# Kernel tuning notes

Measured on AMD Instinct MI355X. Metric: run time of the kernel, lower is better.

Reference implementation:

```python
import jax, jax.numpy as jnp
import numpy as np

NUM_HEADS = 12
HEAD_SIZE = 64  # hidden_size // num_heads


def setup_inputs() -> dict:
    key = jax.random.key(0)
    ks = jax.random.split(key, 4)
    B, S, H = 2, 2048, 768
    return {
        "hidden_states": jax.random.normal(ks[0], (B, S, H), dtype=jnp.float32),
        "attention_mask": jnp.ones((B, S), dtype=jnp.int32),
        "Wq": jax.random.normal(ks[1], (H, H), dtype=jnp.float32) * 0.02,
        "bq": jnp.zeros((H,), dtype=jnp.float32),
        "Wk": jax.random.normal(ks[2], (H, H), dtype=jnp.float32) * 0.02,
        "bk": jnp.zeros((H,), dtype=jnp.float32),
        "Wv": jax.random.normal(ks[3], (H, H), dtype=jnp.float32) * 0.02,
        "bv": jnp.zeros((H,), dtype=jnp.float32),
    }


def reference(hidden_states, attention_mask, Wq, bq, Wk, bk, Wv, bv):
    B, S, H = hidden_states.shape
    nh, hs = NUM_HEADS, HEAD_SIZE

    def to_heads(x):  # [B,S,H] -> [nh,B,S,hs] (matches to_multi_head)
        return x.reshape(B, S, nh, hs).transpose(2, 0, 1, 3)

    # torch Linear: y = x @ W.T + b
    q = to_heads(hidden_states @ Wq.T + bq)
    k = to_heads(hidden_states @ Wk.T + bk)
    v = to_heads(hidden_states @ Wv.T + bv)

    scores = jnp.einsum("hbqd,hbkd->hbqk", q, k) / jnp.float32(hs) ** 0.5
    # mask: 1 -> attend, 0 -> -inf; broadcast over query dim
    m = 1.0 - attention_mask.astype(scores.dtype)
    add = jnp.where(m != 0.0, -jnp.inf, 0.0)[None, :, None, :]  # [1,B,1,S]
    probs = jax.nn.softmax(scores + add, axis=-1)
    # dropout is identity in eval mode
    out = jnp.einsum("hbqk,hbkd->hbqd", probs, v)
    # from_multi_head: [nh,B,S,hs] -> [B,S,H]
    return out.transpose(1, 2, 0, 3).reshape(B, S, H)
```

## Files before the change

kernel.cpp:

```cpp
#include <hip/hip_runtime.h>
#include <hip/hip_bf16.h>

#define BATCH 2
#define SEQ   2048
#define HID   768
#define NH    12
#define HS    64
#define MROWS (BATCH*SEQ)
#define N3    (3*HID)
#define HB    (NH*BATCH)

typedef __attribute__((ext_vector_type(8))) short short8;
typedef __attribute__((ext_vector_type(4))) float floatx4;

#define QSCALE 0.1803368801111204f

__device__ __forceinline__ unsigned short f2bf(float x){
  __hip_bfloat16 h = __float2bfloat16(x);
  return __builtin_bit_cast(unsigned short, h);
}
__device__ __forceinline__ unsigned int f2bf2(float lo, float hi){
  return (unsigned int)f2bf(lo) | ((unsigned int)f2bf(hi) << 16);
}
__device__ __forceinline__ void glds16(const unsigned short* g, unsigned short* l){
  __builtin_amdgcn_global_load_lds(
    (const __attribute__((address_space(1))) unsigned int*)g,
    (__attribute__((address_space(3))) unsigned int*)l, 16, 0, 0);
}

__global__ void f2bf_all_kernel(const float* __restrict__ X,
                                const float* __restrict__ Wq,
                                const float* __restrict__ Wk,
                                const float* __restrict__ Wv,
                                const int* __restrict__ mask,
                                unsigned short* __restrict__ Xb,
                                unsigned short* __restrict__ Wb,
                                float* __restrict__ maskaddG,
                                int* __restrict__ flagsG){
  const int XQ = MROWS*HID/4;
  const int WQ = HID*HID/4;
  const int NB = (XQ + 3*WQ)/256;
  const int tid = threadIdx.x;
  if(blockIdx.x == NB){
    for(int i=tid;i<BATCH*SEQ;i+=256) maskaddG[i] = mask[i] ? 0.f : -1e30f;
    if(tid < BATCH*32){
      int b = tid >> 5, t = tid & 31;
      const int* mrow = mask + b*SEQ + t*64;
      int any = 0;
      for(int i=0;i<64;i++) any |= (mrow[i]==0);
      flagsG[tid] = any;
    }
    return;
  }
  int i = blockIdx.x * 256 + tid;
  const float* src; unsigned short* dst; int off;
  if(i < XQ){ src = X; dst = Xb; off = i; }
  else {
    int j = i - XQ;
    int w = j / WQ; off = j - w*WQ;
    src = (w==0) ? Wq : (w==1) ? Wk : Wv;
    dst = Wb + (size_t)w*HID*HID;
  }
  float4 v = reinterpret_cast<const float4*>(src)[off];
  ushort4 o;
  o.x = f2bf(v.x); o.y = f2bf(v.y); o.z = f2bf(v.z); o.w = f2bf(v.w);
  reinterpret_cast<ushort4*>(dst)[off] = o;
}

__global__ __launch_bounds__(256) void qkv_gemm_kernel(
    const unsigned short* __restrict__ Xb,
    const unsigned short* __restrict__ Wb,
    const float* __restrict__ bq, const float* __restrict__ bk, const float* __restrict__ bv,
    unsigned short* __restrict__ Qb, unsigned short* __restrict__ Kb,
    unsigned short* __restrict__ Vtb)
{
  __shared__ __align__(16) union {
    struct { unsigned short A[2][128][32]; unsigned short B[2][128][32]; } s;
    unsigned short T[4][64][72];
  } u;
  const int m0 = blockIdx.y << 7;
  const int n0 = blockIdx.x << 7;
  const int tid  = threadIdx.x;
  const int wave = tid >> 6, lane = tid & 63;
  const int wr = wave >> 1, wc = wave & 1;
  const int quad = lane >> 4, l15 = lane & 15;

  const unsigned short* gsrc[4];
  unsigned short* ldst[4];
  #pragma unroll
  for(int p=0;p<4;p++){
    int ck  = ((p&1)<<8) + tid;
    int row = ck>>2, c = ck&3, pc = c ^ (row&3);
    if(p<2){ gsrc[p] = Xb + (size_t)(m0+row)*HID + (pc<<3); ldst[p] = &u.s.A[0][row][c<<3]; }
    else   { gsrc[p] = Wb + (size_t)(n0+row)*HID + (pc<<3); ldst[p] = &u.s.B[0][row][c<<3]; }
  }

  floatx4 acc[4][4];
  #pragma unroll
  for(int i=0;i<4;i++)
    #pragma unroll
    for(int j=0;j<4;j++) acc[i][j] = (floatx4){0.f,0.f,0.f,0.f};

  auto stage = [&](int buf, int k0){
    const int bo = buf*(128*32);
    #pragma unroll
    for(int p=0;p<4;p++) glds16(gsrc[p] + k0, ldst[p] + bo);
  };

  stage(0, 0);
  __syncthreads();

  const int swa = l15 & 3;
  for(int t=0;t<HID/32;t++){
    const int buf = t & 1;
    if(t < HID/32 - 1) stage(buf^1, (t+1)*32);
    short8 a[4], b[4];
    #pragma unroll
    for(int i=0;i<4;i++)
      a[i] = *reinterpret_cast<const short8*>(&u.s.A[buf][wr*64+i*16+l15][(quad^swa)<<3]);
    #pragma unroll
    for(int j=0;j<4;j++)
      b[j] = *reinterpret_cast<const short8*>(&u.s.B[buf][wc*64+j*16+l15][(quad^swa)<<3]);
    #pragma unroll
    for(int i=0;i<4;i++)
      #pragma unroll
      for(int j=0;j<4;j++)
        acc[i][j] = __builtin_amdgcn_mfma_f32_16x16x32_bf16(a[i], b[j], acc[i][j], 0, 0, 0);
    __syncthreads();
  }

  const int which = n0 / HID;
  const int nbase = n0 - which*HID + wc*64;
  const int head  = nbase >> 6;
  const int b_    = m0 >> 11;
  const int hb    = head*BATCH + b_;
  const int s0    = (m0 & 2047) + wr*64;
  if(which < 2){
    unsigned short* dst = which==0 ? Qb : Kb;
    const float* bias = which==0 ? bq : bk;
    const float scale = which==0 ? QSCALE : 1.0f;
    #pragma unroll
    for(int j=0;j<4;j++){
      const float bb = bias[nbase + j*16 + l15];
      #pragma unroll
      for(int i=0;i<4;i++)
        #pragma unroll
        for(int r=0;r<4;r++)
          u.T[wave][i*16 + quad*4 + r][j*16 + l15] = f2bf((acc[i][j][r] + bb)*scale);
    }
    #pragma unroll
    for(int p=0;p<8;p++){
      const int row = p*8 + (lane>>3), dc = (lane&7)*8;
      uint4 v = *reinterpret_cast<const uint4*>(&u.T[wave][row][dc]);
      *reinterpret_cast<uint4*>(dst + ((size_t)(hb<<11) + s0 + row)*HS + dc) = v;
    }
  } else {
    #pragma unroll
    for(int j=0;j<4;j++){
      const float bb = bv[nbase + j*16 + l15];
      #pragma unroll
      for(int i=0;i<4;i++){
        uint2 pk;
        pk.x = f2bf2(acc[i][j][0]+bb, acc[i][j][1]+bb);
        pk.y = f2bf2(acc[i][j][2]+bb, acc[i][j][3]+bb);
        *reinterpret_cast<uint2*>(&u.T[wave][j*16+l15][i*16 + quad*4]) = pk;
      }
    }
    #pragma unroll
    for(int p=0;p<8;p++){
      const int d = p*8 + (lane>>3), cm = lane & 7;
      uint4 v = *reinterpret_cast<const uint4*>(&u.T[wave][d][cm*8]);
      *reinterpret_cast<uint4*>(Vtb + ((size_t)(hb*HS) + d)*SEQ + s0 + cm*8) = v;
    }
  }
}

__global__ __launch_bounds__(256) void attn_kernel(
    const unsigned short* __restrict__ Qb,
    const unsigned short* __restrict__ Kb,
    const unsigned short* __restrict__ Vtb,
    const float* __restrict__ maskaddG,
    const int* __restrict__ flagsG,
    float* __restrict__ out)
{
  __shared__ __align__(16) unsigned short Ks2 [2][64][64];
  __shared__ __align__(16) unsigned short Vts2[2][64][64];
  __shared__ __align__(16) unsigned short Ps2 [4][16][68];

  const int bid = blockIdx.x;
  const int hb = bid >> 5, qt = bid & 31, q0 = qt << 6;
  const int tid = threadIdx.x, wave = tid >> 6, lane = tid & 63;
  const int quad = lane >> 4, l15 = lane & 15;
  const int b_ = hb & 1, head = hb >> 1;

  const unsigned short* gK[2]; const unsigned short* gV[2];
  unsigned short* lK[2]; unsigned short* lV[2];
  #pragma unroll
  for(int p=0;p<2;p++){
    int ck = (p<<8) + tid;
    int row = ck>>3, c = ck&7, pc = c ^ (row&7);
    gK[p] = Kb  + ((size_t)(hb<<11) + row)*HS + (pc<<3);
    lK[p] = &Ks2[0][row][c<<3];
    gV[p] = Vtb + ((size_t)(hb*HS) + row)*SEQ + (pc<<3);
    lV[p] = &Vts2[0][row][c<<3];
  }
  auto stage = [&](int buf, int k0){
    const int bo = buf*(64*64);
    #pragma unroll
    for(int p=0;p<2;p++){
      glds16(gK[p] + (size_t)k0*HS, lK[p] + bo);
      glds16(gV[p] + k0,           lV[p] + bo);
    }
  };

  stage(0, 0);

  short8 a_q[2];
  {
    const unsigned short* qsrc = Qb + ((size_t)(hb<<11) + q0 + wave*16 + l15)*HS;
    a_q[0] = *reinterpret_cast<const short8*>(qsrc + quad*8);
    a_q[1] = *reinterpret_cast<const short8*>(qsrc + 32 + quad*8);
  }

  float lsum4[4] = {0.f,0.f,0.f,0.f};
  floatx4 o_acc[4];
  #pragma unroll
  for(int dt=0;dt<4;dt++) o_acc[dt] = (floatx4){0.f,0.f,0.f,0.f};

  __syncthreads();

  const int sw = l15 & 7;
  for(int t=0;t<SEQ/64;t++){
    const int buf = t & 1, k0 = t << 6;
    if(t < SEQ/64 - 1) stage(buf^1, k0 + 64);

    const unsigned short (*Kst)[64] = Ks2[buf];
    const unsigned short (*Vst)[64] = Vts2[buf];

    floatx4 st[4];
    #pragma unroll
    for(int kt=0;kt<4;kt++){
      st[kt] = (floatx4){0.f,0.f,0.f,0.f};
      #pragma unroll
      for(int c=0;c<2;c++){
        short8 kf = *reinterpret_cast<const short8*>(
            &Kst[kt*16 + l15][(((c<<2)+quad)^sw)<<3]);
        st[kt] = __builtin_amdgcn_mfma_f32_16x16x32_bf16(kf, a_q[c], st[kt], 0, 0, 0);
      }
    }

    const bool masked = (flagsG[(b_<<5) + t] != 0);
    #pragma unroll
    for(int kt=0;kt<4;kt++){
      float p0,p1,p2,p3;
      if(!masked){
        p0 = exp2f(st[kt][0]); p1 = exp2f(st[kt][1]);
        p2 = exp2f(st[kt][2]); p3 = exp2f(st[kt][3]);
      } else {
        float4 ma = *reinterpret_cast<const float4*>(
            maskaddG + (b_<<11) + k0 + kt*16 + quad*4);
        p0 = exp2f(st[kt][0] + ma.x); p1 = exp2f(st[kt][1] + ma.y);
        p2 = exp2f(st[kt][2] + ma.z); p3 = exp2f(st[kt][3] + ma.w);
      }
      lsum4[0] += p0; lsum4[1] += p1; lsum4[2] += p2; lsum4[3] += p3;
      uint2 pk;
      pk.x = f2bf2(p0, p1);
      pk.y = f2bf2(p2, p3);
      *reinterpret_cast<uint2*>(&Ps2[wave][l15][kt*16 + quad*4]) = pk;
    }

    short8 ap0, ap1;
    {
      unsigned long long x0 = *reinterpret_cast<const unsigned long long*>(&Ps2[wave][l15][quad*8]);
      unsigned long long x1 = *reinterpret_cast<const unsigned long long*>(&Ps2[wave][l15][quad*8 + 4]);
      unsigned long long y0 = *reinterpret_cast<const unsigned long long*>(&Ps2[wave][l15][32 + quad*8]);
      unsigned long long y1 = *reinterpret_cast<const unsigned long long*>(&Ps2[wave][l15][32 + quad*8 + 4]);
      union { unsigned long long u[2]; short8 s; } cv0, cv1;
      cv0.u[0] = x0; cv0.u[1] = x1;
      cv1.u[0] = y0; cv1.u[1] = y1;
      ap0 = cv0.s; ap1 = cv1.s;
    }
    #pragma unroll
    for(int dt=0;dt<4;dt++){
      short8 bv0 = *reinterpret_cast<const short8*>(&Vst[dt*16 + l15][(quad^sw)<<3]);
      short8 bv1 = *reinterpret_cast<const short8*>(&Vst[dt*16 + l15][((4+quad)^sw)<<3]);
      o_acc[dt] = __builtin_amdgcn_mfma_f32_16x16x32_bf16(ap0, bv0, o_acc[dt], 0, 0, 0);
      o_acc[dt] = __builtin_amdgcn_mfma_f32_16x16x32_bf16(ap1, bv1, o_acc[dt], 0, 0, 0);
    }
    __syncthreads();
  }

  float lsum = (lsum4[0]+lsum4[1]) + (lsum4[2]+lsum4[3]);
  lsum += __shfl_xor(lsum, 16);
  lsum += __shfl_xor(lsum, 32);
  float linv[4];
  #pragma unroll
  for(int r=0;r<4;r++) linv[r] = 1.0f / __shfl(lsum, quad*4 + r);

  #pragma unroll
  for(int dt=0;dt<4;dt++){
    #pragma unroll
    for(int r=0;r<4;r++){
      const int srow = q0 + wave*16 + quad*4 + r;
      out[((size_t)(b_<<11) + srow)*HID + (head<<6) + dt*16 + l15] =
        o_acc[dt][r] * linv[r];
    }
  }
}

extern "C" void kernel_launch(void* const* d_in, const int* in_sizes, int n_in,
                              void* d_out, int out_size, void* d_ws, size_t ws_size,
                              hipStream_t stream) {
  const float* X    = (const float*)d_in[0];
  const int*   mask = (const int*)  d_in[1];
  const float* Wq   = (const float*)d_in[2];
  const float* bq   = (const float*)d_in[3];
  const float* Wk   = (const float*)d_in[4];
  const float* bk   = (const float*)d_in[5];
  const float* Wv   = (const float*)d_in[6];
  const float* bv   = (const float*)d_in[7];
  float* out = (float*)d_out;

  char* ws = (char*)d_ws;
  unsigned short* Xb  = (unsigned short*)ws;
  unsigned short* Wb  = Xb  + (size_t)MROWS*HID;
  unsigned short* Qb  = Wb  + (size_t)N3*HID;
  unsigned short* Kb  = Qb  + (size_t)HB*SEQ*HS;
  unsigned short* Vtb = Kb  + (size_t)HB*SEQ*HS;
  float* maskaddG = (float*)(Vtb + (size_t)HB*SEQ*HS);
  int*   flagsG   = (int*)(maskaddG + MROWS);

  const int total_quads = (MROWS*HID + 3*HID*HID)/4;
  f2bf_all_kernel<<<total_quads/256 + 1, 256, 0, stream>>>(
      X, Wq, Wk, Wv, mask, Xb, Wb, maskaddG, flagsG);

  qkv_gemm_kernel<<<dim3(N3/128, MROWS/128), 256, 0, stream>>>(
      Xb, Wb, bq, bk, bv, Qb, Kb, Vtb);

  attn_kernel<<<HB*32, 256, 0, stream>>>(
      Qb, Kb, Vtb, maskaddG, flagsG, out);
}
```

Before: 175.2 us.

## Add producer wave for K/V loads with LDS flag handshakes instead of barriers

The attention kernel gets a fifth wave that acts as a dedicated producer. It streams K and V^T tiles into a double-buffered LDS area and signals readiness through workgroup-scope atomic flags. The four consumer waves spin on those flags and report completion per buffer, replacing the per-iteration __syncthreads. Mask flags are also packed into one bitmask word per batch, so each tile needs a bit test instead of a global load. The risks are spin-wait overhead, lower occupancy from 320-thread blocks, and the producer running only one tile ahead.

```diff
diff --git a/kernel.cpp b/kernel.cpp
--- a/kernel.cpp
+++ b/kernel.cpp
@@ -27,6 +27,7 @@
     (const __attribute__((address_space(1))) unsigned int*)g,
     (__attribute__((address_space(3))) unsigned int*)l, 16, 0, 0);
 }
+#define WAITCNT_VM_LGKM0() __builtin_amdgcn_s_waitcnt(0x0070)
 
 __global__ void f2bf_all_kernel(const float* __restrict__ X,
                                 const float* __restrict__ Wq,
@@ -36,19 +37,21 @@
                                 unsigned short* __restrict__ Xb,
                                 unsigned short* __restrict__ Wb,
                                 float* __restrict__ maskaddG,
-                                int* __restrict__ flagsG){
+                                unsigned int* __restrict__ flagsG){
   const int XQ = MROWS*HID/4;
   const int WQ = HID*HID/4;
   const int NB = (XQ + 3*WQ)/256;
   const int tid = threadIdx.x;
   if(blockIdx.x == NB){
     for(int i=tid;i<BATCH*SEQ;i+=256) maskaddG[i] = mask[i] ? 0.f : -1e30f;
+    if(tid < 2) flagsG[tid] = 0u;
+    __syncthreads();
     if(tid < BATCH*32){
       int b = tid >> 5, t = tid & 31;
       const int* mrow = mask + b*SEQ + t*64;
       int any = 0;
       for(int i=0;i<64;i++) any |= (mrow[i]==0);
-      flagsG[tid] = any;
+      if(any) atomicOr(&flagsG[b], 1u << t);
     }
     return;
   }
@@ -175,45 +178,56 @@
   }
 }
 
-__global__ __launch_bounds__(256) void attn_kernel(
+__global__ __launch_bounds__(320) void attn_kernel(
     const unsigned short* __restrict__ Qb,
     const unsigned short* __restrict__ Kb,
     const unsigned short* __restrict__ Vtb,
     const float* __restrict__ maskaddG,
-    const int* __restrict__ flagsG,
+    const unsigned int* __restrict__ flagsG,
     float* __restrict__ out)
 {
   __shared__ __align__(16) unsigned short Ks2 [2][64][64];
   __shared__ __align__(16) unsigned short Vts2[2][64][64];
   __shared__ __align__(16) unsigned short Ps2 [4][16][68];
+  __shared__ int ready[2];
+  __shared__ int done[2];
 
   const int bid = blockIdx.x;
   const int hb = bid >> 5, qt = bid & 31, q0 = qt << 6;
   const int tid = threadIdx.x, wave = tid >> 6, lane = tid & 63;
   const int quad = lane >> 4, l15 = lane & 15;
   const int b_ = hb & 1, head = hb >> 1;
-
-  const unsigned short* gK[2]; const unsigned short* gV[2];
-  unsigned short* lK[2]; unsigned short* lV[2];
-  #pragma unroll
-  for(int p=0;p<2;p++){
-    int ck = (p<<8) + tid;
-    int row = ck>>3, c = ck&7, pc = c ^ (row&7);
-    gK[p] = Kb  + ((size_t)(hb<<11) + row)*HS + (pc<<3);
-    lK[p] = &Ks2[0][row][c<<3];
-    gV[p] = Vtb + ((size_t)(hb*HS) + row)*SEQ + (pc<<3);
-    lV[p] = &Vts2[0][row][c<<3];
-  }
-  auto stage = [&](int buf, int k0){
-    const int bo = buf*(64*64);
-    #pragma unroll
-    for(int p=0;p<2;p++){
-      glds16(gK[p] + (size_t)k0*HS, lK[p] + bo);
-      glds16(gV[p] + k0,           lV[p] + bo);
-    }
-  };
-
-  stage(0, 0);
+  const int NT = SEQ/64;
+
+  if(tid < 2){ ready[tid] = -1; done[tid] = 0; }
+  __syncthreads();
+
+  if(wave == 4){
+    const int prow = lane >> 3;
+    const int pcol = lane & 7;
+    const int ppc  = pcol ^ prow;
+    const unsigned short* gK0 = Kb  + ((size_t)(hb<<11) + prow)*HS + (ppc<<3);
+    const unsigned short* gV0 = Vtb + ((size_t)(hb*HS) + prow)*SEQ + (ppc<<3);
+
+    for(int t=0;t<NT;t++){
+      const int b = t & 1, k0 = t << 6;
+      const int k = (t - b) >> 1;
+      if(k > 0){
+        while(__hip_atomic_load(&done[b], __ATOMIC_ACQUIRE, __HIP_MEMORY_SCOPE_WORKGROUP) < 4*k)
+          __builtin_amdgcn_s_sleep(1);
+      }
+      #pragma unroll
+      for(int p=0;p<8;p++)
+        glds16(gK0 + (size_t)(k0 + p*8)*HS, &Ks2[b][p*8 + prow][pcol*8]);
+      #pragma unroll
+      for(int p=0;p<8;p++)
+        glds16(gV0 + (size_t)(p*8)*SEQ + k0, &Vts2[b][p*8 + prow][pcol*8]);
+      WAITCNT_VM_LGKM0();
+      if(lane == 0)
+        __hip_atomic_store(&ready[b], t, __ATOMIC_RELEASE, __HIP_MEMORY_SCOPE_WORKGROUP);
+    }
+    return;
+  }
 
   short8 a_q[2];
   {
@@ -221,21 +235,21 @@
     a_q[0] = *reinterpret_cast<const short8*>(qsrc + quad*8);
     a_q[1] = *reinterpret_cast<const short8*>(qsrc + 32 + quad*8);
   }
+  const unsigned int fl = flagsG[b_];
 
   float lsum4[4] = {0.f,0.f,0.f,0.f};
   floatx4 o_acc[4];
   #pragma unroll
   for(int dt=0;dt<4;dt++) o_acc[dt] = (floatx4){0.f,0.f,0.f,0.f};
 
-  __syncthreads();
-
   const int sw = l15 & 7;
-  for(int t=0;t<SEQ/64;t++){
-    const int buf = t & 1, k0 = t << 6;
-    if(t < SEQ/64 - 1) stage(buf^1, k0 + 64);
-
-    const unsigned short (*Kst)[64] = Ks2[buf];
-    const unsigned short (*Vst)[64] = Vts2[buf];
+  for(int t=0;t<NT;t++){
+    const int b = t & 1, k0 = t << 6;
+    while(__hip_atomic_load(&ready[b], __ATOMIC_ACQUIRE, __HIP_MEMORY_SCOPE_WORKGROUP) < t)
+      __builtin_amdgcn_s_sleep(1);
+
+    const unsigned short (*Kst)[64] = Ks2[b];
+    const unsigned short (*Vst)[64] = Vts2[b];
 
     floatx4 st[4];
     #pragma unroll
@@ -249,7 +263,7 @@
       }
     }
 
-    const bool masked = (flagsG[(b_<<5) + t] != 0);
+    const bool masked = (fl >> t) & 1u;
     #pragma unroll
     for(int kt=0;kt<4;kt++){
       float p0,p1,p2,p3;
@@ -287,7 +301,10 @@
       o_acc[dt] = __builtin_amdgcn_mfma_f32_16x16x32_bf16(ap0, bv0, o_acc[dt], 0, 0, 0);
       o_acc[dt] = __builtin_amdgcn_mfma_f32_16x16x32_bf16(ap1, bv1, o_acc[dt], 0, 0, 0);
     }
-    __syncthreads();
+
+    WAITCNT_VM_LGKM0();
+    if(lane == 0)
+      __hip_atomic_fetch_add(&done[b], 1, __ATOMIC_RELEASE, __HIP_MEMORY_SCOPE_WORKGROUP);
   }
 
   float lsum = (lsum4[0]+lsum4[1]) + (lsum4[2]+lsum4[3]);
@@ -328,7 +345,7 @@
   unsigned short* Kb  = Qb  + (size_t)HB*SEQ*HS;
   unsigned short* Vtb = Kb  + (size_t)HB*SEQ*HS;
   float* maskaddG = (float*)(Vtb + (size_t)HB*SEQ*HS);
-  int*   flagsG   = (int*)(maskaddG + MROWS);
+  unsigned int* flagsG = (unsigned int*)(maskaddG + MROWS);
 
   const int total_quads = (MROWS*HID + 3*HID*HID)/4;
   f2bf_all_kernel<<<total_quads/256 + 1, 256, 0, stream>>>(
@@ -337,6 +354,6 @@
   qkv_gemm_kernel<<<dim3(N3/128, MROWS/128), 256, 0, stream>>>(
       Xb, Wb, bq, bk, bv, Qb, Kb, Vtb);
 
-  attn_kernel<<<HB*32, 256, 0, stream>>>(
+  attn_kernel<<<HB*32, 320, 0, stream>>>(
       Qb, Kb, Vtb, maskaddG, flagsG, out);
 }
```

After: 175.5 us. No clear change (+0.2%).

## Fuse bf16 conversion into QKV GEMM via grid-wide barrier, pack mask flags

Applied to the files above, without the earlier changes.

Merges the fp32-to-bf16 conversion kernel into the QKV GEMM kernel. All 576 blocks first do a grid-stride conversion, then synchronize through a global atomic spin barrier before starting the GEMM. Mask flags become one bitmask word per batch, loaded once per attention block instead of once per tile. The probability packing switches to a cheaper round-half-up bit trick. This removes a kernel launch and a per-tile global load, but the barrier only works if all 576 blocks are resident at once (launch_bounds 256,3) and adds a memset launch.

```diff
diff --git a/kernel.cpp b/kernel.cpp
--- a/kernel.cpp
+++ b/kernel.cpp
@@ -9,6 +9,7 @@
 #define MROWS (BATCH*SEQ)
 #define N3    (3*HID)
 #define HB    (NH*BATCH)
+#define NBLK_GEMM 576
 
 typedef __attribute__((ext_vector_type(8))) short short8;
 typedef __attribute__((ext_vector_type(4))) float floatx4;
@@ -21,6 +22,11 @@
 }
 __device__ __forceinline__ unsigned int f2bf2(float lo, float hi){
   return (unsigned int)f2bf(lo) | ((unsigned int)f2bf(hi) << 16);
+}
+__device__ __forceinline__ unsigned int f2bf2_rhu(float lo, float hi){
+  unsigned int a = __builtin_bit_cast(unsigned int, lo) + 0x8000u;
+  unsigned int b = __builtin_bit_cast(unsigned int, hi) + 0x8000u;
+  return __builtin_amdgcn_perm(b, a, 0x07060302u);
 }
 __device__ __forceinline__ void glds16(const unsigned short* g, unsigned short* l){
   __builtin_amdgcn_global_load_lds(
@@ -28,59 +34,69 @@
     (__attribute__((address_space(3))) unsigned int*)l, 16, 0, 0);
 }
 
-__global__ void f2bf_all_kernel(const float* __restrict__ X,
-                                const float* __restrict__ Wq,
-                                const float* __restrict__ Wk,
-                                const float* __restrict__ Wv,
-                                const int* __restrict__ mask,
-                                unsigned short* __restrict__ Xb,
-                                unsigned short* __restrict__ Wb,
-                                float* __restrict__ maskaddG,
-                                int* __restrict__ flagsG){
-  const int XQ = MROWS*HID/4;
-  const int WQ = HID*HID/4;
-  const int NB = (XQ + 3*WQ)/256;
+__global__ __launch_bounds__(256, 3) void qkv_fused_kernel(
+    const float* __restrict__ X,
+    const float* __restrict__ Wq, const float* __restrict__ Wk, const float* __restrict__ Wv,
+    const int* __restrict__ mask,
+    const float* __restrict__ bq, const float* __restrict__ bk, const float* __restrict__ bv,
+    unsigned short* __restrict__ Xb,
+    unsigned short* __restrict__ Wb,
+    unsigned short* __restrict__ Qb, unsigned short* __restrict__ Kb,
+    unsigned short* __restrict__ Vtb,
+    float* __restrict__ maskaddG, unsigned int* __restrict__ flagsG,
+    unsigned int* __restrict__ bar)
+{
   const int tid = threadIdx.x;
-  if(blockIdx.x == NB){
-    for(int i=tid;i<BATCH*SEQ;i+=256) maskaddG[i] = mask[i] ? 0.f : -1e30f;
-    if(tid < BATCH*32){
-      int b = tid >> 5, t = tid & 31;
-      const int* mrow = mask + b*SEQ + t*64;
-      int any = 0;
-      for(int i=0;i<64;i++) any |= (mrow[i]==0);
-      flagsG[tid] = any;
-    }
-    return;
-  }
-  int i = blockIdx.x * 256 + tid;
-  const float* src; unsigned short* dst; int off;
-  if(i < XQ){ src = X; dst = Xb; off = i; }
-  else {
-    int j = i - XQ;
-    int w = j / WQ; off = j - w*WQ;
-    src = (w==0) ? Wq : (w==1) ? Wk : Wv;
-    dst = Wb + (size_t)w*HID*HID;
-  }
-  float4 v = reinterpret_cast<const float4*>(src)[off];
-  ushort4 o;
-  o.x = f2bf(v.x); o.y = f2bf(v.y); o.z = f2bf(v.z); o.w = f2bf(v.w);
-  reinterpret_cast<ushort4*>(dst)[off] = o;
-}
-
-__global__ __launch_bounds__(256) void qkv_gemm_kernel(
-    const unsigned short* __restrict__ Xb,
-    const unsigned short* __restrict__ Wb,
-    const float* __restrict__ bq, const float* __restrict__ bk, const float* __restrict__ bv,
-    unsigned short* __restrict__ Qb, unsigned short* __restrict__ Kb,
-    unsigned short* __restrict__ Vtb)
-{
+  const int bid = blockIdx.y * gridDim.x + blockIdx.x;
+
+  {
+    const int XQ = MROWS*HID/4;
+    const int WQ = HID*HID/4;
+    const int TOT = XQ + 3*WQ;
+    for(int i = bid*256 + tid; i < TOT; i += NBLK_GEMM*256){
+      const float* src; unsigned short* dst; int off;
+      if(i < XQ){ src = X; dst = Xb; off = i; }
+      else {
+        int j = i - XQ;
+        int w = j / WQ; off = j - w*WQ;
+        src = (w==0) ? Wq : (w==1) ? Wk : Wv;
+        dst = Wb + (size_t)w*HID*HID;
+      }
+      float4 v = reinterpret_cast<const float4*>(src)[off];
+      ushort4 o;
+      o.x = f2bf(v.x); o.y = f2bf(v.y); o.z = f2bf(v.z); o.w = f2bf(v.w);
+      reinterpret_cast<ushort4*>(dst)[off] = o;
+    }
+    if(bid == 0){
+      for(int i=tid;i<BATCH*SEQ;i+=256) maskaddG[i] = mask[i] ? 0.f : -1e30f;
+      if(tid < 2) flagsG[tid] = 0u;
+      __syncthreads();
+      if(tid < BATCH*32){
+        int b = tid >> 5, t = tid & 31;
+        const int* mrow = mask + b*SEQ + t*64;
+        int any = 0;
+        for(int i=0;i<64;i++) any |= (mrow[i]==0);
+        if(any) atomicOr(&flagsG[b], 1u << t);
+      }
+    }
+  }
+
+  __syncthreads();
+  if(tid == 0){
+    __threadfence();
+    __hip_atomic_fetch_add(bar, 1u, __ATOMIC_RELEASE, __HIP_MEMORY_SCOPE_AGENT);
+    while(__hip_atomic_load(bar, __ATOMIC_ACQUIRE, __HIP_MEMORY_SCOPE_AGENT) < NBLK_GEMM)
+      __builtin_amdgcn_s_sleep(2);
+    __threadfence();
+  }
+  __syncthreads();
+
   __shared__ __align__(16) union {
     struct { unsigned short A[2][128][32]; unsigned short B[2][128][32]; } s;
     unsigned short T[4][64][72];
   } u;
   const int m0 = blockIdx.y << 7;
   const int n0 = blockIdx.x << 7;
-  const int tid  = threadIdx.x;
   const int wave = tid >> 6, lane = tid & 63;
   const int wr = wave >> 1, wc = wave & 1;
   const int quad = lane >> 4, l15 = lane & 15;
@@ -180,7 +196,7 @@
     const unsigned short* __restrict__ Kb,
     const unsigned short* __restrict__ Vtb,
     const float* __restrict__ maskaddG,
-    const int* __restrict__ flagsG,
+    const unsigned int* __restrict__ flagsG,
     float* __restrict__ out)
 {
   __shared__ __align__(16) unsigned short Ks2 [2][64][64];
@@ -221,6 +237,7 @@
     a_q[0] = *reinterpret_cast<const short8*>(qsrc + quad*8);
     a_q[1] = *reinterpret_cast<const short8*>(qsrc + 32 + quad*8);
   }
+  const unsigned int fl = flagsG[b_];
 
   float lsum4[4] = {0.f,0.f,0.f,0.f};
   floatx4 o_acc[4];
@@ -249,7 +266,7 @@
       }
     }
 
-    const bool masked = (flagsG[(b_<<5) + t] != 0);
+    const bool masked = (fl >> t) & 1u;
     #pragma unroll
     for(int kt=0;kt<4;kt++){
       float p0,p1,p2,p3;
@@ -264,8 +281,8 @@
       }
       lsum4[0] += p0; lsum4[1] += p1; lsum4[2] += p2; lsum4[3] += p3;
       uint2 pk;
-      pk.x = f2bf2(p0, p1);
-      pk.y = f2bf2(p2, p3);
+      pk.x = f2bf2_rhu(p0, p1);
+      pk.y = f2bf2_rhu(p2, p3);
       *reinterpret_cast<uint2*>(&Ps2[wave][l15][kt*16 + quad*4]) = pk;
     }
 
@@ -328,14 +345,14 @@
   unsigned short* Kb  = Qb  + (size_t)HB*SEQ*HS;
   unsigned short* Vtb = Kb  + (size_t)HB*SEQ*HS;
   float* maskaddG = (float*)(Vtb + (size_t)HB*SEQ*HS);
-  int*   flagsG   = (int*)(maskaddG + MROWS);
-
-  const int total_quads = (MROWS*HID + 3*HID*HID)/4;
-  f2bf_all_kernel<<<total_quads/256 + 1, 256, 0, stream>>>(
-      X, Wq, Wk, Wv, mask, Xb, Wb, maskaddG, flagsG);
-
-  qkv_gemm_kernel<<<dim3(N3/128, MROWS/128), 256, 0, stream>>>(
-      Xb, Wb, bq, bk, bv, Qb, Kb, Vtb);
+  unsigned int* flagsG = (unsigned int*)(maskaddG + MROWS);
+  unsigned int* bar    = (unsigned int*)(((uintptr_t)(flagsG + 2) + 63) & ~(uintptr_t)63);
+
+  hipMemsetAsync(bar, 0, 64, stream);
+
+  qkv_fused_kernel<<<dim3(N3/128, MROWS/128), 256, 0, stream>>>(
+      X, Wq, Wk, Wv, mask, bq, bk, bv,
+      Xb, Wb, Qb, Kb, Vtb, maskaddG, flagsG, bar);
 
   attn_kernel<<<HB*32, 256, 0, stream>>>(
       Qb, Kb, Vtb, maskaddG, flagsG, out);
```

Result: slower. 267.3 us (+52.6%).
